# Performance work log

Measured on AMD Instinct MI355X. Metric: run time of the kernel, lower is better.

The kernel has to match this reference:

```python
import jax, jax.numpy as jnp
import numpy as np

LMAX = 5
DIMS = [2 * l + 1 for l in range(LMAX + 1)]
S = sum(d * d for d in DIMS)  # 286 = sum_l (2l+1)^2 (mul_l = dim_l = 2l+1)
F_IN, F_OUT = 128, 128
B = 512
N_GRID = 512


def setup_inputs() -> dict:
    key = jax.random.key(0)
    k1, k2, k3 = jax.random.split(key, 3)
    # x: signal over SO(3) irreps, shape (B, f_in, S)
    x = jax.random.normal(k1, (B, F_IN, S), dtype=jnp.float32)
    # w: learned spatial filter, shape (f_in, f_out, n_grid) (nn.Parameter, normal init)
    w = jax.random.normal(k2, (F_IN, F_OUT, N_GRID), dtype=jnp.float32)
    # D: flattened Wigner-D buffer, shape (n_grid, S). Stand-in random values;
    # the forward math is identical to the true Wigner-D buffer.
    D = jax.random.normal(k3, (N_GRID, S), dtype=jnp.float32)
    return {"x": x, "w": w, "D": D}


def _so3_linear(x, psi):
    """e3nn o3.Linear over so3_irreps(LMAX) with external weights psi.

    Per degree l: x_l (B, f_in, 2l+1 [mul], 2l+1 [dim]),
    psi_l (f_in, f_out, mul_in, mul_out); mix multiplicities and f channels,
    with fan-in normalization 1/sqrt(f_in * mul_in).
    """
    bsz = x.shape[0]
    outs = []
    off = 0
    for l in range(LMAX + 1):
        d = 2 * l + 1
        blk = d * d
        x_l = x[:, :, off:off + blk].reshape(bsz, F_IN, d, d)
        w_l = psi[:, :, off:off + blk].reshape(F_IN, F_OUT, d, d)
        scale = 1.0 / np.sqrt(F_IN * d).astype(np.float32)
        y_l = jnp.einsum('bxui,xyuv->byvi', x_l, w_l) * scale
        outs.append(y_l.reshape(bsz, F_OUT, blk))
        off += blk
    return jnp.concatenate(outs, axis=-1)


def reference(x, w, D):
    # project spatial filter into harmonic (Fourier) domain
    psi = jnp.einsum('ni,xyn->xyi', D, w) / np.float32(np.sqrt(N_GRID))
    return _so3_linear(x, psi)
```

## Files before the change

### kernel.cpp

```cpp
#include <hip/hip_runtime.h>
#include <hip/hip_bf16.h>


#define NT 256
#define NTILES 1144
#define NWORKERS 768
typedef __bf16 bf16x8 __attribute__((ext_vector_type(8)));
typedef float f32x4 __attribute__((ext_vector_type(4)));
typedef unsigned int u32;

__device__ __forceinline__ void gload_lds16(const void* g, void* l) {
  __builtin_amdgcn_global_load_lds(
      (const __attribute__((address_space(1))) u32*)g,
      (__attribute__((address_space(3))) u32*)l, 16, 0, 0);
}

__device__ __forceinline__ void decode_s(int s, int& off, int& d) {
  if (s >= 165)      { off = 165; d = 11; }
  else if (s >= 84)  { off = 84;  d = 9; }
  else if (s >= 35)  { off = 35;  d = 7; }
  else if (s >= 10)  { off = 10;  d = 5; }
  else if (s >= 1)   { off = 1;   d = 3; }
  else               { off = 0;   d = 1; }
}

template<int D, int OFF>
__device__ __forceinline__ void build_one(const float* __restrict__ X,
                                          __hip_bfloat16* __restrict__ A,
                                          int b, __hip_bfloat16* sm) {
  const float* src = X + (size_t)b * (128 * 286) + OFF;
  for (int e = threadIdx.x; e < 128 * D * D; e += NT) {
    const int x = e / (D * D), r = e - x * (D * D);
    sm[e] = __float2bfloat16(src[x * 286 + r]);
  }
  __syncthreads();
  __hip_bfloat16* dst = A + (size_t)65536 * OFF + (size_t)b * (D * 128 * D);
  for (int o = threadIdx.x; o < D * 128 * D; o += NT) {
    const int i = o / (128 * D);
    const int rem = o - i * (128 * D);
    const int x = rem / D, u = rem - x * D;
    dst[o] = sm[x * D * D + u * D + i];
  }
}

__global__ __launch_bounds__(NT)
void prep_all(const float* __restrict__ w, const float* __restrict__ Dm,
              const float* __restrict__ X,
              __hip_bfloat16* __restrict__ wb, __hip_bfloat16* __restrict__ DT,
              __hip_bfloat16* __restrict__ A, int* __restrict__ cnt) {
  __shared__ __hip_bfloat16 sm[128 * 121];
  const int bx = blockIdx.x;
  if (bx == 0 && threadIdx.x == 0) *cnt = 0;
  if (bx < 4096) {
    const int t = bx * NT + threadIdx.x;
    const float4 a = reinterpret_cast<const float4*>(w)[t * 2];
    const float4 b = reinterpret_cast<const float4*>(w)[t * 2 + 1];
    __hip_bfloat16 v[8];
    v[0] = __float2bfloat16(a.x); v[1] = __float2bfloat16(a.y);
    v[2] = __float2bfloat16(a.z); v[3] = __float2bfloat16(a.w);
    v[4] = __float2bfloat16(b.x); v[5] = __float2bfloat16(b.y);
    v[6] = __float2bfloat16(b.z); v[7] = __float2bfloat16(b.w);
    *reinterpret_cast<bf16x8*>(&wb[t * 8]) = *reinterpret_cast<bf16x8*>(v);
  } else if (bx < 4864) {
    const int e = (bx - 4096) * NT + threadIdx.x;
    const int s = e >> 9, g = e & 511;
    DT[e] = (s < 286) ? __float2bfloat16(Dm[g * 286 + s]) : __float2bfloat16(0.0f);
  } else {
    const int b2 = bx - 4864;
    if (b2 < 512)       build_one<11, 165>(X, A, b2, sm);
    else if (b2 < 1024) build_one<9, 84>(X, A, b2 - 512, sm);
    else if (b2 < 1536) build_one<7, 35>(X, A, b2 - 1024, sm);
    else if (b2 < 2048) build_one<5, 10>(X, A, b2 - 1536, sm);
    else if (b2 < 2560) build_one<3, 1>(X, A, b2 - 2048, sm);
    else                build_one<1, 0>(X, A, b2 - 2560, sm);
  }
}

__device__ __forceinline__ void stage_tile(
    const __hip_bfloat16* __restrict__ Ap, const __hip_bfloat16* __restrict__ Bp,
    int LDK, int ktv, int m0, int n0, int tid, int wave,
    __hip_bfloat16* sA, __hip_bfloat16* sB) {
#pragma unroll
  for (int c = 0; c < 4; ++c) {
    const int q = c * 256 + tid;
    const int row = q >> 3, slot = q & 7;
    const int scol = ((slot ^ (row & 7)) << 3);
    gload_lds16(&Ap[(m0 + row) * LDK + ktv + scol], &sA[(c * 256 + wave * 64) << 3]);
    gload_lds16(&Bp[(n0 + row) * LDK + ktv + scol], &sB[(c * 256 + wave * 64) << 3]);
  }
}

__device__ __forceinline__ void load_frags(
    const __hip_bfloat16* sA, const __hip_bfloat16* sB,
    int wr, int wc, int r15, int khi, bf16x8 (&af)[4][2], bf16x8 (&bf)[4][2]) {
#pragma unroll
  for (int m = 0; m < 4; ++m)
#pragma unroll
    for (int kk = 0; kk < 2; ++kk) {
      const int row = wr * 64 + m * 16 + r15;
      const int slot = (kk * 4 + khi) ^ (row & 7);
      af[m][kk] = *reinterpret_cast<const bf16x8*>(&sA[row * 64 + slot * 8]);
    }
#pragma unroll
  for (int n = 0; n < 4; ++n)
#pragma unroll
    for (int kk = 0; kk < 2; ++kk) {
      const int row = wc * 64 + n * 16 + r15;
      const int slot = (kk * 4 + khi) ^ (row & 7);
      bf[n][kk] = *reinterpret_cast<const bf16x8*>(&sB[row * 64 + slot * 8]);
    }
}

__device__ __forceinline__ void do_mfma(
    const bf16x8 (&af)[4][2], const bf16x8 (&bf)[4][2], f32x4 (&acc)[4][4]) {
#pragma unroll
  for (int kk = 0; kk < 2; ++kk)
#pragma unroll
    for (int m = 0; m < 4; ++m)
#pragma unroll
      for (int n = 0; n < 4; ++n)
        acc[m][n] = __builtin_amdgcn_mfma_f32_16x16x32_bf16(
            af[m][kk], bf[n][kk], acc[m][n], 0, 0, 0);
}

__global__ __launch_bounds__(NT)
void psi_mfma(const __hip_bfloat16* __restrict__ wb,
              const __hip_bfloat16* __restrict__ DT,
              __hip_bfloat16* __restrict__ PT) {
  const int m0 = blockIdx.x * 128, n0 = blockIdx.y * 128;

  __shared__ __hip_bfloat16 sA[2][128 * 64];
  __shared__ __hip_bfloat16 sB[2][128 * 64];

  const int tid = threadIdx.x;
  const int lane = tid & 63, wave = tid >> 6;
  const int wr = wave & 1, wc = wave >> 1;
  const int r15 = lane & 15, khi = lane >> 4;

  f32x4 acc[4][4] = {};
  bf16x8 af[4][2], bf[4][2];

  stage_tile(wb, DT, 512, 0, m0, n0, tid, wave, sA[0], sB[0]);
  __syncthreads();
  int cur = 0;
  for (int t = 0; t < 8; ++t) {
    if (t + 1 < 8)
      stage_tile(wb, DT, 512, (t + 1) << 6, m0, n0, tid, wave, sA[cur ^ 1], sB[cur ^ 1]);
    load_frags(sA[cur], sB[cur], wr, wc, r15, khi, af, bf);
    do_mfma(af, bf, acc);
    if (t + 1 < 8) { __syncthreads(); cur ^= 1; }
  }

#pragma unroll
  for (int n = 0; n < 4; ++n) {
    const int s = n0 + wc * 64 + n * 16 + r15;
    if (s >= 286) continue;
    int off, d;
    decode_s(s, off, d);
    const int rel = s - off;
    const int u = rel / d, v = rel - u * d;
    const float scale = 1.0f / (256.0f * sqrtf((float)d));
    __hip_bfloat16* Pl = PT + off * 16384;
    const int Kd = 128 * d;
#pragma unroll
    for (int m = 0; m < 4; ++m)
#pragma unroll
      for (int j = 0; j < 4; ++j) {
        const int row = m0 + wr * 64 + m * 16 + khi * 4 + j;
        const int x = row >> 7, y = row & 127;
        Pl[(y * d + v) * Kd + (x * d + u)] = __float2bfloat16(acc[m][n][j] * scale);
      }
  }
}

template<int D, int OFF>
__device__ __forceinline__ void tile_body(
    const __hip_bfloat16* __restrict__ Aall,
    const __hip_bfloat16* __restrict__ PTall,
    float* __restrict__ out, int bx,
    __hip_bfloat16* sA, __hip_bfloat16* sB, float* sE) {
  const int tid = threadIdx.x;
  const int lane = tid & 63, wave = tid >> 6;
  const int wr = wave & 1, wc = wave >> 1;
  const int r15 = lane & 15, khi = lane >> 4;

  constexpr int Kn = 128 * D;
  constexpr int nk = 2 * D;
  const int bm = bx % (4 * D);
  const int bn = bx / (4 * D);
  const __hip_bfloat16* A  = Aall  + 65536 * OFF;
  const __hip_bfloat16* BT = PTall + 16384 * OFF;
  const int m0 = bm * 128, n0 = bn * 128;

  f32x4 acc[4][4] = {};
  bf16x8 af[4][2], bf[4][2];

  for (int t = 0; t < nk; ++t) {
    const int kt = t << 6;
#pragma unroll
    for (int c = 0; c < 4; ++c) {
      const int q = c * 256 + tid;
      const int row = q >> 3, slot = q & 7;
      const int scol = ((slot ^ (row & 7)) << 3);
      gload_lds16(&A[(m0 + row) * Kn + kt + scol], &sA[(c * 256 + wave * 64) << 3]);
      gload_lds16(&BT[(n0 + row) * Kn + kt + scol], &sB[(c * 256 + wave * 64) << 3]);
    }
    __syncthreads();
    load_frags(sA, sB, wr, wc, r15, khi, af, bf);
    do_mfma(af, bf, acc);
    __syncthreads();
  }

#pragma unroll
  for (int ch = 0; ch < 2; ++ch) {
    if (wr == ch) {
#pragma unroll
      for (int m = 0; m < 4; ++m)
#pragma unroll
        for (int j = 0; j < 4; ++j) {
          const int lr = m * 16 + khi * 4 + j;
#pragma unroll
          for (int n = 0; n < 4; ++n) {
            const int c = wc * 64 + n * 16 + r15;
            sE[lr * 129 + c] = acc[m][n][j];
          }
        }
    }
    __syncthreads();
    const int base_row = m0 + ch * 64;
    const int b_lo = base_row / D;
    const int yo_lo = n0 / D;
    constexpr int NBMAX = 64 / D + 2;
    constexpr int NYOC = 128 / D + 2;
    constexpr int TOT = NBMAX * NYOC * D * D;
    for (int e = tid; e < TOT; e += NT) {
      const int s = e % (D * D);
      const int t2 = e / (D * D);
      const int yos = t2 % NYOC;
      const int bs = t2 / NYOC;
      const int b = b_lo + bs;
      const int yo = yo_lo + yos;
      const int i = s % D, v = s / D;
      const int row = b * D + i;
      const int col = yo * D + v;
      if (row < base_row || row >= base_row + 64) continue;
      if (col < n0 || col >= n0 + 128) continue;
      out[(size_t)b * 36608 + yo * 286 + OFF + v * D + i] =
          sE[(row - base_row) * 129 + (col - n0)];
    }
    __syncthreads();
  }
}

__global__ __launch_bounds__(NT)
void main_gemm(const __hip_bfloat16* __restrict__ Aall,
               const __hip_bfloat16* __restrict__ PTall,
               float* __restrict__ out, int* __restrict__ cnt) {
  __shared__ __align__(16) unsigned char smem[33024];
  __shared__ int s_tile;
  __hip_bfloat16* sA = (__hip_bfloat16*)smem;
  __hip_bfloat16* sB = (__hip_bfloat16*)(smem + 16384);
  float* sE = (float*)smem;

  for (;;) {
    if (threadIdx.x == 0) s_tile = atomicAdd(cnt, 1);
    __syncthreads();
    const int bx = s_tile;
    if (bx >= NTILES) return;
    if (bx < 484)       tile_body<11, 165>(Aall, PTall, out, bx, sA, sB, sE);
    else if (bx < 808)  tile_body<9, 84>(Aall, PTall, out, bx - 484, sA, sB, sE);
    else if (bx < 1004) tile_body<7, 35>(Aall, PTall, out, bx - 808, sA, sB, sE);
    else if (bx < 1104) tile_body<5, 10>(Aall, PTall, out, bx - 1004, sA, sB, sE);
    else if (bx < 1140) tile_body<3, 1>(Aall, PTall, out, bx - 1104, sA, sB, sE);
    else                tile_body<1, 0>(Aall, PTall, out, bx - 1140, sA, sB, sE);
  }
}

extern "C" void kernel_launch(void* const* d_in, const int* in_sizes, int n_in,
                              void* d_out, int out_size, void* d_ws, size_t ws_size,
                              hipStream_t stream) {
  const float* x  = (const float*)d_in[0];
  const float* w  = (const float*)d_in[1];
  const float* Dm = (const float*)d_in[2];
  float* out = (float*)d_out;

  __hip_bfloat16* PT = (__hip_bfloat16*)d_ws;
  __hip_bfloat16* A  = PT + 16384 * 286;
  __hip_bfloat16* wb = A + 65536 * 286;
  __hip_bfloat16* DT = wb + 16384 * 512;
  int* cnt = (int*)(DT + 384 * 512);

  prep_all<<<dim3(7936), dim3(NT), 0, stream>>>(w, Dm, x, wb, DT, A, cnt);
  psi_mfma<<<dim3(128, 3), dim3(NT), 0, stream>>>(wb, DT, PT);
  main_gemm<<<dim3(NWORKERS), dim3(NT), 0, stream>>>(A, PT, out, cnt);
}
```

Before: 179.4 us.

## Double-buffer main GEMM LDS loads, store epilogue directly, drop persistent tile scheduler

```diff
diff --git a/kernel.cpp b/kernel.cpp
--- a/kernel.cpp
+++ b/kernel.cpp
@@ -3,8 +3,6 @@
 
 
 #define NT 256
-#define NTILES 1144
-#define NWORKERS 768
 typedef __bf16 bf16x8 __attribute__((ext_vector_type(8)));
 typedef float f32x4 __attribute__((ext_vector_type(4)));
 typedef unsigned int u32;
@@ -47,10 +45,9 @@
 void prep_all(const float* __restrict__ w, const float* __restrict__ Dm,
               const float* __restrict__ X,
               __hip_bfloat16* __restrict__ wb, __hip_bfloat16* __restrict__ DT,
-              __hip_bfloat16* __restrict__ A, int* __restrict__ cnt) {
+              __hip_bfloat16* __restrict__ A) {
   __shared__ __hip_bfloat16 sm[128 * 121];
   const int bx = blockIdx.x;
-  if (bx == 0 && threadIdx.x == 0) *cnt = 0;
   if (bx < 4096) {
     const int t = bx * NT + threadIdx.x;
     const float4 a = reinterpret_cast<const float4*>(w)[t * 2];
@@ -76,6 +73,39 @@
   }
 }
 
+__device__ __forceinline__ void load_frags(
+    const __hip_bfloat16* sA, const __hip_bfloat16* sB,
+    int wr, int wc, int r15, int khi, bf16x8 (&af)[4][2], bf16x8 (&bf)[4][2]) {
+#pragma unroll
+  for (int m = 0; m < 4; ++m)
+#pragma unroll
+    for (int kk = 0; kk < 2; ++kk) {
+      const int row = wr * 64 + m * 16 + r15;
+      const int slot = (kk * 4 + khi) ^ (row & 7);
+      af[m][kk] = *reinterpret_cast<const bf16x8*>(&sA[row * 64 + slot * 8]);
+    }
+#pragma unroll
+  for (int n = 0; n < 4; ++n)
+#pragma unroll
+    for (int kk = 0; kk < 2; ++kk) {
+      const int row = wc * 64 + n * 16 + r15;
+      const int slot = (kk * 4 + khi) ^ (row & 7);
+      bf[n][kk] = *reinterpret_cast<const bf16x8*>(&sB[row * 64 + slot * 8]);
+    }
+}
+
+__device__ __forceinline__ void do_mfma(
+    const bf16x8 (&af)[4][2], const bf16x8 (&bf)[4][2], f32x4 (&acc)[4][4]) {
+#pragma unroll
+  for (int kk = 0; kk < 2; ++kk)
+#pragma unroll
+    for (int m = 0; m < 4; ++m)
+#pragma unroll
+      for (int n = 0; n < 4; ++n)
+        acc[m][n] = __builtin_amdgcn_mfma_f32_16x16x32_bf16(
+            af[m][kk], bf[n][kk], acc[m][n], 0, 0, 0);
+}
+
 __device__ __forceinline__ void stage_tile(
     const __hip_bfloat16* __restrict__ Ap, const __hip_bfloat16* __restrict__ Bp,
     int LDK, int ktv, int m0, int n0, int tid, int wave,
@@ -88,39 +118,6 @@
     gload_lds16(&Ap[(m0 + row) * LDK + ktv + scol], &sA[(c * 256 + wave * 64) << 3]);
     gload_lds16(&Bp[(n0 + row) * LDK + ktv + scol], &sB[(c * 256 + wave * 64) << 3]);
   }
-}
-
-__device__ __forceinline__ void load_frags(
-    const __hip_bfloat16* sA, const __hip_bfloat16* sB,
-    int wr, int wc, int r15, int khi, bf16x8 (&af)[4][2], bf16x8 (&bf)[4][2]) {
-#pragma unroll
-  for (int m = 0; m < 4; ++m)
-#pragma unroll
-    for (int kk = 0; kk < 2; ++kk) {
-      const int row = wr * 64 + m * 16 + r15;
-      const int slot = (kk * 4 + khi) ^ (row & 7);
-      af[m][kk] = *reinterpret_cast<const bf16x8*>(&sA[row * 64 + slot * 8]);
-    }
-#pragma unroll
-  for (int n = 0; n < 4; ++n)
-#pragma unroll
-    for (int kk = 0; kk < 2; ++kk) {
-      const int row = wc * 64 + n * 16 + r15;
-      const int slot = (kk * 4 + khi) ^ (row & 7);
-      bf[n][kk] = *reinterpret_cast<const bf16x8*>(&sB[row * 64 + slot * 8]);
-    }
-}
-
-__device__ __forceinline__ void do_mfma(
-    const bf16x8 (&af)[4][2], const bf16x8 (&bf)[4][2], f32x4 (&acc)[4][4]) {
-#pragma unroll
-  for (int kk = 0; kk < 2; ++kk)
-#pragma unroll
-    for (int m = 0; m < 4; ++m)
-#pragma unroll
-      for (int n = 0; n < 4; ++n)
-        acc[m][n] = __builtin_amdgcn_mfma_f32_16x16x32_bf16(
-            af[m][kk], bf[n][kk], acc[m][n], 0, 0, 0);
 }
 
 __global__ __launch_bounds__(NT)
@@ -178,7 +175,8 @@
     const __hip_bfloat16* __restrict__ Aall,
     const __hip_bfloat16* __restrict__ PTall,
     float* __restrict__ out, int bx,
-    __hip_bfloat16* sA, __hip_bfloat16* sB, float* sE) {
+    __hip_bfloat16* s0A, __hip_bfloat16* s0B,
+    __hip_bfloat16* s1A, __hip_bfloat16* s1B) {
   const int tid = threadIdx.x;
   const int lane = tid & 63, wave = tid >> 6;
   const int wr = wave & 1, wc = wave >> 1;
@@ -192,88 +190,83 @@
   const __hip_bfloat16* BT = PTall + 16384 * OFF;
   const int m0 = bm * 128, n0 = bn * 128;
 
+  const int q0 = tid;
   f32x4 acc[4][4] = {};
   bf16x8 af[4][2], bf[4][2];
 
+  __hip_bfloat16 *curA = s0A, *curB = s0B, *nxtA = s1A, *nxtB = s1B;
+
+#pragma unroll
+  for (int c = 0; c < 4; ++c) {
+    const int q = c * 256 + q0;
+    const int row = q >> 3, slot = q & 7;
+    const int scol = ((slot ^ (row & 7)) << 3);
+    gload_lds16(&A[(m0 + row) * Kn + scol], &curA[(c * 256 + wave * 64) << 3]);
+    gload_lds16(&BT[(n0 + row) * Kn + scol], &curB[(c * 256 + wave * 64) << 3]);
+  }
+
   for (int t = 0; t < nk; ++t) {
-    const int kt = t << 6;
-#pragma unroll
-    for (int c = 0; c < 4; ++c) {
-      const int q = c * 256 + tid;
-      const int row = q >> 3, slot = q & 7;
-      const int scol = ((slot ^ (row & 7)) << 3);
-      gload_lds16(&A[(m0 + row) * Kn + kt + scol], &sA[(c * 256 + wave * 64) << 3]);
-      gload_lds16(&BT[(n0 + row) * Kn + kt + scol], &sB[(c * 256 + wave * 64) << 3]);
-    }
-    __syncthreads();
-    load_frags(sA, sB, wr, wc, r15, khi, af, bf);
+    if (t + 1 < nk) {
+      const int kt = (t + 1) << 6;
+#pragma unroll
+      for (int c = 0; c < 4; ++c) {
+        const int q = c * 256 + q0;
+        const int row = q >> 3, slot = q & 7;
+        const int scol = ((slot ^ (row & 7)) << 3);
+        gload_lds16(&A[(m0 + row) * Kn + kt + scol], &nxtA[(c * 256 + wave * 64) << 3]);
+        gload_lds16(&BT[(n0 + row) * Kn + kt + scol], &nxtB[(c * 256 + wave * 64) << 3]);
+      }
+      asm volatile("s_waitcnt vmcnt(8)" ::: "memory");
+    } else {
+      asm volatile("s_waitcnt vmcnt(0)" ::: "memory");
+    }
+    __builtin_amdgcn_s_barrier();
+    asm volatile("" ::: "memory");
+
+    load_frags(curA, curB, wr, wc, r15, khi, af, bf);
+    __builtin_amdgcn_s_setprio(1);
     do_mfma(af, bf, acc);
-    __syncthreads();
-  }
-
-#pragma unroll
-  for (int ch = 0; ch < 2; ++ch) {
-    if (wr == ch) {
-#pragma unroll
-      for (int m = 0; m < 4; ++m)
-#pragma unroll
-        for (int j = 0; j < 4; ++j) {
-          const int lr = m * 16 + khi * 4 + j;
-#pragma unroll
-          for (int n = 0; n < 4; ++n) {
-            const int c = wc * 64 + n * 16 + r15;
-            sE[lr * 129 + c] = acc[m][n][j];
-          }
-        }
-    }
-    __syncthreads();
-    const int base_row = m0 + ch * 64;
-    const int b_lo = base_row / D;
-    const int yo_lo = n0 / D;
-    constexpr int NBMAX = 64 / D + 2;
-    constexpr int NYOC = 128 / D + 2;
-    constexpr int TOT = NBMAX * NYOC * D * D;
-    for (int e = tid; e < TOT; e += NT) {
-      const int s = e % (D * D);
-      const int t2 = e / (D * D);
-      const int yos = t2 % NYOC;
-      const int bs = t2 / NYOC;
-      const int b = b_lo + bs;
-      const int yo = yo_lo + yos;
-      const int i = s % D, v = s / D;
-      const int row = b * D + i;
-      const int col = yo * D + v;
-      if (row < base_row || row >= base_row + 64) continue;
-      if (col < n0 || col >= n0 + 128) continue;
-      out[(size_t)b * 36608 + yo * 286 + OFF + v * D + i] =
-          sE[(row - base_row) * 129 + (col - n0)];
-    }
-    __syncthreads();
-  }
+    __builtin_amdgcn_s_setprio(0);
+
+    asm volatile("" ::: "memory");
+    __builtin_amdgcn_s_barrier();
+    __hip_bfloat16* tA = curA; curA = nxtA; nxtA = tA;
+    __hip_bfloat16* tB = curB; curB = nxtB; nxtB = tB;
+  }
+
+  int yo4[4], v4[4];
+#pragma unroll
+  for (int n = 0; n < 4; ++n) {
+    const int col = n0 + wc * 64 + n * 16 + r15;
+    yo4[n] = col / D;
+    v4[n] = col - yo4[n] * D;
+  }
+#pragma unroll
+  for (int m = 0; m < 4; ++m)
+#pragma unroll
+    for (int j = 0; j < 4; ++j) {
+      const int row = m0 + wr * 64 + m * 16 + khi * 4 + j;
+      const int bb = row / D, i = row - bb * D;
+      float* orow = out + (size_t)bb * 36608 + OFF + i;
+#pragma unroll
+      for (int n = 0; n < 4; ++n)
+        orow[yo4[n] * 286 + v4[n] * D] = acc[m][n][j];
+    }
 }
 
 __global__ __launch_bounds__(NT)
 void main_gemm(const __hip_bfloat16* __restrict__ Aall,
                const __hip_bfloat16* __restrict__ PTall,
-               float* __restrict__ out, int* __restrict__ cnt) {
-  __shared__ __align__(16) unsigned char smem[33024];
-  __shared__ int s_tile;
-  __hip_bfloat16* sA = (__hip_bfloat16*)smem;
-  __hip_bfloat16* sB = (__hip_bfloat16*)(smem + 16384);
-  float* sE = (float*)smem;
-
-  for (;;) {
-    if (threadIdx.x == 0) s_tile = atomicAdd(cnt, 1);
-    __syncthreads();
-    const int bx = s_tile;
-    if (bx >= NTILES) return;
-    if (bx < 484)       tile_body<11, 165>(Aall, PTall, out, bx, sA, sB, sE);
-    else if (bx < 808)  tile_body<9, 84>(Aall, PTall, out, bx - 484, sA, sB, sE);
-    else if (bx < 1004) tile_body<7, 35>(Aall, PTall, out, bx - 808, sA, sB, sE);
-    else if (bx < 1104) tile_body<5, 10>(Aall, PTall, out, bx - 1004, sA, sB, sE);
-    else if (bx < 1140) tile_body<3, 1>(Aall, PTall, out, bx - 1104, sA, sB, sE);
-    else                tile_body<1, 0>(Aall, PTall, out, bx - 1140, sA, sB, sE);
-  }
+               float* __restrict__ out) {
+  __shared__ __hip_bfloat16 sA[2][128 * 64];
+  __shared__ __hip_bfloat16 sB[2][128 * 64];
+  const int bx = blockIdx.x;
+  if (bx < 484)       tile_body<11, 165>(Aall, PTall, out, bx,        sA[0], sB[0], sA[1], sB[1]);
+  else if (bx < 808)  tile_body<9, 84>(Aall, PTall, out, bx - 484,   sA[0], sB[0], sA[1], sB[1]);
+  else if (bx < 1004) tile_body<7, 35>(Aall, PTall, out, bx - 808,   sA[0], sB[0], sA[1], sB[1]);
+  else if (bx < 1104) tile_body<5, 10>(Aall, PTall, out, bx - 1004,  sA[0], sB[0], sA[1], sB[1]);
+  else if (bx < 1140) tile_body<3, 1>(Aall, PTall, out, bx - 1104,   sA[0], sB[0], sA[1], sB[1]);
+  else                tile_body<1, 0>(Aall, PTall, out, bx - 1140,   sA[0], sB[0], sA[1], sB[1]);
 }
 
 extern "C" void kernel_launch(void* const* d_in, const int* in_sizes, int n_in,
@@ -288,9 +281,8 @@
   __hip_bfloat16* A  = PT + 16384 * 286;
   __hip_bfloat16* wb = A + 65536 * 286;
   __hip_bfloat16* DT = wb + 16384 * 512;
-  int* cnt = (int*)(DT + 384 * 512);
-
-  prep_all<<<dim3(7936), dim3(NT), 0, stream>>>(w, Dm, x, wb, DT, A, cnt);
+
+  prep_all<<<dim3(7936), dim3(NT), 0, stream>>>(w, Dm, x, wb, DT, A);
   psi_mfma<<<dim3(128, 3), dim3(NT), 0, stream>>>(wb, DT, PT);
-  main_gemm<<<dim3(NWORKERS), dim3(NT), 0, stream>>>(A, PT, out, cnt);
-}
+  main_gemm<<<dim3(1144), dim3(NT), 0, stream>>>(A, PT, out);
+}
```

Result: faster. 164.2 us (-8.5%).
